# Kernel optimization log

Hardware: AMD Instinct MI355X
Metric: run time of the kernel (lower is better)

The kernel has to match this reference:

```python
import jax, jax.numpy as jnp
import numpy as np

TOP_K = 8


def setup_inputs() -> dict:
    key = jax.random.key(0)
    ks = jax.random.split(key, 10)
    B, N, F = 16, 4096, 256
    M = 4096  # memory_size
    s = 1.0 / np.sqrt(F)
    return {
        "query": jax.random.normal(ks[0], (B, N, F), jnp.float32),
        "memory_keys": jax.random.normal(ks[1], (M, F), jnp.float32),
        "memory_values": jax.random.normal(ks[2], (M, F), jnp.float32),
        "Wq": jax.random.normal(ks[3], (F, F), jnp.float32) * s,
        "bq": jnp.zeros((F,), jnp.float32),
        "W1": jax.random.normal(ks[4], (2 * F, F), jnp.float32) * (1.0 / np.sqrt(2 * F)),
        "b1": jnp.zeros((F,), jnp.float32),
        "W2": jax.random.normal(ks[5], (F, F), jnp.float32) * s,
        "b2": jnp.zeros((F,), jnp.float32),
    }


def reference(query, memory_keys, memory_values, Wq, bq, W1, b1, W2, b2):
    # query: (B, N, F)
    q = jnp.einsum("bnf,fg->bng", query, Wq) + bq
    # similarity vs memory bank: (B, N, M)
    sim = jnp.einsum("bnf,mf->bnm", q, memory_keys)
    topk_sim, topk_idx = jax.lax.top_k(sim, TOP_K)          # (B, N, K)
    topk_values = memory_values[topk_idx]                    # (B, N, K, F) gather
    weights = jax.nn.softmax(topk_sim, axis=-1)[..., None]   # (B, N, K, 1)
    retrieved = jnp.sum(topk_values * weights, axis=-2)      # (B, N, F)
    h = jnp.concatenate([query, retrieved], axis=-1)         # (B, N, 2F)
    h = jax.nn.relu(jnp.einsum("bnf,fg->bng", h, W1) + b1)
    out = jnp.einsum("bnf,fg->bng", h, W2) + b2
    return out
```

## Files before the change

### kernel.cpp

```cpp
#include <hip/hip_runtime.h>

typedef _Float16 f16x8 __attribute__((ext_vector_type(8)));
typedef _Float16 f16x4 __attribute__((ext_vector_type(4)));
typedef float f32x4 __attribute__((ext_vector_type(4)));

#define BN   65536
#define MSZ  4096
#define TOPK 8

#define MFMA(a, b, c) __builtin_amdgcn_mfma_f32_16x16x32_f16(a, b, c, 0, 0, 0)

__global__ void cvt_f16(const float* __restrict__ src, _Float16* __restrict__ dst,
                        int n) {
    int i = blockIdx.x * 256 + threadIdx.x;
    if (i < n) dst[i] = (_Float16)src[i];
}

__global__ void cvt_transpose(const float* __restrict__ src, _Float16* __restrict__ dst,
                              int K, int N) {
    int i = blockIdx.x * 256 + threadIdx.x;
    if (i < K * N) {
        int k = i / N, n = i - k * N;
        dst[n * K + k] = (_Float16)src[i];
    }
}

__device__ __forceinline__ unsigned pack_key(float s, unsigned inv12) {
    unsigned u = __float_as_uint(s);
    unsigned m = (unsigned)(((int)u) >> 31) | 0x80000000u;
    unsigned k = u ^ m;
    return (k & 0xFFFFF000u) | inv12;
}

__device__ __forceinline__ unsigned med3u(unsigned a, unsigned b, unsigned c) {
    unsigned d;
    asm("v_med3_u32 %0, %1, %2, %3" : "=v"(d) : "v"(a), "v"(b), "v"(c));
    return d;
}

template <int N>
__device__ __forceinline__ void ins(unsigned* t, unsigned key) {
#pragma unroll
    for (int p = N - 1; p > 0; --p) t[p] = med3u(t[p - 1], t[p], key);
    t[0] = (t[0] > key) ? t[0] : key;
}

__device__ __forceinline__ int swz(int r, int cb) {
    return (r << 9) + (cb ^ ((r & 7) << 4));
}

__global__ __launch_bounds__(256, 2) void fused_all(
        const float*    __restrict__ query,
        const _Float16* __restrict__ keysH,
        const float*    __restrict__ vals,
        const _Float16* __restrict__ WqT,
        const float*    __restrict__ bq,
        const _Float16* __restrict__ W1T,
        const float*    __restrict__ b1,
        const _Float16* __restrict__ W2T,
        const float*    __restrict__ b2,
        float* __restrict__ out)
{
    __shared__ __attribute__((aligned(16))) unsigned char SM[65536];
    unsigned char* const SA = SM;
    unsigned char* const SB = SM + 32768;

    const int tid  = threadIdx.x;
    const int lane = tid & 63, quad = lane >> 4, l16 = lane & 15, wave = tid >> 6;
    const size_t row0 = (size_t)blockIdx.x * 64;

#pragma unroll
    for (int j = 0; j < 8; ++j) {
        int u = (j << 8) + tid;
        int r = u >> 5, f = (u & 31) << 3;
        float4 x = *(const float4*)(query + (row0 + r) * 256 + f);
        float4 y = *(const float4*)(query + (row0 + r) * 256 + f + 4);
        f16x8 h = {(_Float16)x.x, (_Float16)x.y, (_Float16)x.z, (_Float16)x.w,
                   (_Float16)y.x, (_Float16)y.y, (_Float16)y.z, (_Float16)y.w};
        *(f16x8*)(SA + swz(r, f << 1)) = h;
    }
    __syncthreads();

    {
        f32x4 acc[4][4];
#pragma unroll
        for (int rt = 0; rt < 4; ++rt)
#pragma unroll
            for (int nt = 0; nt < 4; ++nt)
                acc[rt][nt] = (f32x4){0.f, 0.f, 0.f, 0.f};
#pragma unroll
        for (int kf = 0; kf < 8; ++kf) {
            f16x8 a[4];
#pragma unroll
            for (int rt = 0; rt < 4; ++rt)
                a[rt] = *(const f16x8*)(SA + swz(rt * 16 + l16, kf * 64 + quad * 16));
#pragma unroll
            for (int nt = 0; nt < 4; ++nt) {
                int n0 = wave * 16 + nt * 64;
                f16x8 b = *(const f16x8*)(WqT + (size_t)(n0 + l16) * 256 + kf * 32 + quad * 8);
#pragma unroll
                for (int rt = 0; rt < 4; ++rt)
                    acc[rt][nt] = MFMA(a[rt], b, acc[rt][nt]);
            }
        }
#pragma unroll
        for (int nt = 0; nt < 4; ++nt) {
            int col = wave * 16 + nt * 64 + l16;
            float bv = bq[col];
#pragma unroll
            for (int rt = 0; rt < 4; ++rt)
#pragma unroll
                for (int r = 0; r < 4; ++r) {
                    int row = rt * 16 + quad * 4 + r;
                    *(_Float16*)(SB + swz(row, col * 2)) =
                        (_Float16)(acc[rt][nt][r] + bv);
                }
        }
    }
    __syncthreads();

    f16x8 af[8];
    {
        f16x8 kst[8];
#pragma unroll
        for (int j = 0; j < 8; ++j) {
            int u = (j << 8) + tid;
            int r = u >> 5, cb = (u & 31) << 4;
            kst[j] = *(const f16x8*)((const unsigned char*)keysH + (r << 9) + cb);
        }
#pragma unroll
        for (int nk = 0; nk < 8; ++nk)
            af[nk] = *(const f16x8*)(SB + swz(wave * 16 + l16, nk * 64 + quad * 16));
#pragma unroll
        for (int j = 0; j < 8; ++j) {
            int u = (j << 8) + tid;
            int r = u >> 5, cb = (u & 31) << 4;
            *(f16x8*)(SA + swz(r, cb)) = kst[j];
        }
    }
    __syncthreads();

    unsigned tk[4][7];
#pragma unroll
    for (int s = 0; s < 4; ++s)
#pragma unroll
        for (int e = 0; e < 7; ++e) tk[s][e] = 0u;

#pragma unroll 1
    for (int t = 0; t < 64; ++t) {
        const int cbase = (t & 1) << 15;
        const int nbase = 32768 - cbase;
        const unsigned char* ktg =
            (const unsigned char*)keysH + ((size_t)((t + 1) & 63) << 15);
        f16x8 kst[8];
#pragma unroll
        for (int j = 0; j < 8; ++j) {
            int u = (j << 8) + tid;
            int r = u >> 5, cb = (u & 31) << 4;
            kst[j] = *(const f16x8*)(ktg + (r << 9) + cb);
        }
        const unsigned char* KB = SM + cbase;
#pragma unroll
        for (int n0 = 0; n0 < 64; n0 += 16) {
            f16x8 bf[8];
#pragma unroll
            for (int nk = 0; nk < 8; ++nk)
                bf[nk] = *(const f16x8*)(KB + swz(n0 + l16, nk * 64 + quad * 16));
            f32x4 acc = {0.f, 0.f, 0.f, 0.f};
#pragma unroll
            for (int nk = 0; nk < 8; ++nk) acc = MFMA(af[nk], bf[nk], acc);
            unsigned inv = (~(unsigned)((t << 6) + n0 + l16)) & 0xFFFu;
#pragma unroll
            for (int r = 0; r < 4; ++r) ins<7>(tk[r], pack_key(acc[r], inv));
        }
#pragma unroll
        for (int j = 0; j < 8; ++j) {
            int u = (j << 8) + tid;
            int r = u >> 5, cb = (u & 31) << 4;
            *(f16x8*)(SM + nbase + swz(r, cb)) = kst[j];
        }
        __syncthreads();
    }

    unsigned t8[2][8];
    {
        const int kh = l16 & 1;
#pragma unroll
        for (int j = 0; j < 2; ++j) {
#pragma unroll
            for (int e = 0; e < 7; ++e) t8[j][e] = kh ? tk[2 + j][e] : tk[j][e];
            t8[j][7] = 0u;
        }
#pragma unroll
        for (int j = 0; j < 2; ++j)
#pragma unroll
            for (int e = 0; e < 7; ++e) {
                unsigned snd = kh ? tk[j][e] : tk[2 + j][e];
                unsigned rcv = __shfl_xor(snd, 1);
                ins<8>(t8[j], rcv);
            }
    }
    unsigned keep[8];
    {
        const int k2 = (l16 >> 1) & 1;
        unsigned oth[8];
#pragma unroll
        for (int e = 0; e < 8; ++e) {
            keep[e] = k2 ? t8[1][e] : t8[0][e];
            oth[e]  = k2 ? t8[0][e] : t8[1][e];
        }
#pragma unroll
        for (int e = 0; e < 8; ++e) ins<8>(keep, __shfl_xor(oth[e], 2));
    }
#pragma unroll
    for (int st = 4; st <= 8; st <<= 1) {
        unsigned rcv[8];
#pragma unroll
        for (int e = 0; e < 8; ++e) rcv[e] = __shfl_xor(keep[e], st);
#pragma unroll
        for (int e = 0; e < 8; ++e) ins<8>(keep, rcv[e]);
    }

    int idx[8];
    {
        const int src = ((l16 >> 2) << 4) + (((l16 & 1) << 1) | ((l16 >> 1) & 1));
#pragma unroll
        for (int e = 0; e < 8; ++e) {
            unsigned kb = __shfl(keep[e], src);
            idx[e] = 4095 - (int)(kb & 0xFFFu);
        }
    }

    float wt[8];
    {
        float ps[8];
#pragma unroll
        for (int e = 0; e < 8; ++e) {
            const f16x8* kp = (const f16x8*)(keysH + (size_t)(idx[e] & (MSZ - 1)) * 256);
            float s = 0.f;
#pragma unroll
            for (int nk = 0; nk < 8; ++nk) {
                f16x8 kv = kp[nk * 4 + quad];
                f16x8 qv = af[nk];
#pragma unroll
                for (int i = 0; i < 8; ++i) s += (float)qv[i] * (float)kv[i];
            }
            ps[e] = s;
        }
#pragma unroll
        for (int e = 0; e < 8; ++e) {
            ps[e] += __shfl_xor(ps[e], 16);
            ps[e] += __shfl_xor(ps[e], 32);
        }
        float mx = ps[0];
#pragma unroll
        for (int e = 1; e < 8; ++e) mx = fmaxf(mx, ps[e]);
        float z = 0.f;
#pragma unroll
        for (int e = 0; e < 8; ++e) { wt[e] = __expf(ps[e] - mx); z += wt[e]; }
        float rz = 1.f / z;
#pragma unroll
        for (int e = 0; e < 8; ++e) wt[e] *= rz;
    }

    {
        float rv[64];
#pragma unroll
        for (int i = 0; i < 64; ++i) rv[i] = 0.f;
#pragma unroll
        for (int e = 0; e < 8; ++e) {
            const float4* vp = (const float4*)(vals + (size_t)(idx[e] & (MSZ - 1)) * 256 + quad * 64);
            float w = wt[e];
#pragma unroll
            for (int j = 0; j < 16; ++j) {
                float4 v = vp[j];
                rv[j * 4 + 0] += w * v.x; rv[j * 4 + 1] += w * v.y;
                rv[j * 4 + 2] += w * v.z; rv[j * 4 + 3] += w * v.w;
            }
        }
#pragma unroll
        for (int j = 0; j < 8; ++j) {
            f16x8 h = {(_Float16)rv[j * 8 + 0], (_Float16)rv[j * 8 + 1],
                       (_Float16)rv[j * 8 + 2], (_Float16)rv[j * 8 + 3],
                       (_Float16)rv[j * 8 + 4], (_Float16)rv[j * 8 + 5],
                       (_Float16)rv[j * 8 + 6], (_Float16)rv[j * 8 + 7]};
            *(f16x8*)(SB + swz(wave * 16 + l16, quad * 128 + (j << 4))) = h;
        }
    }
#pragma unroll
    for (int j = 0; j < 8; ++j) {
        int u = (j << 8) + tid;
        int r = u >> 5, f = (u & 31) << 3;
        float4 x = *(const float4*)(query + (row0 + r) * 256 + f);
        float4 y = *(const float4*)(query + (row0 + r) * 256 + f + 4);
        f16x8 h = {(_Float16)x.x, (_Float16)x.y, (_Float16)x.z, (_Float16)x.w,
                   (_Float16)y.x, (_Float16)y.y, (_Float16)y.z, (_Float16)y.w};
        *(f16x8*)(SA + swz(r, f << 1)) = h;
    }
    __syncthreads();

    {
        f32x4 acc[4][4];
#pragma unroll
        for (int rt = 0; rt < 4; ++rt)
#pragma unroll
            for (int nt = 0; nt < 4; ++nt)
                acc[rt][nt] = (f32x4){0.f, 0.f, 0.f, 0.f};
#pragma unroll
        for (int kf = 0; kf < 16; ++kf) {
            const unsigned char* base = (kf < 8) ? SA : SB;
            const int cb = (kf & 7) * 64 + quad * 16;
            f16x8 a[4];
#pragma unroll
            for (int rt = 0; rt < 4; ++rt)
                a[rt] = *(const f16x8*)(base + swz(rt * 16 + l16, cb));
#pragma unroll
            for (int nt = 0; nt < 4; ++nt) {
                int n0 = wave * 16 + nt * 64;
                f16x8 b = *(const f16x8*)(W1T + (size_t)(n0 + l16) * 512 + kf * 32 + quad * 8);
#pragma unroll
                for (int rt = 0; rt < 4; ++rt)
                    acc[rt][nt] = MFMA(a[rt], b, acc[rt][nt]);
            }
        }
        __syncthreads();
#pragma unroll
        for (int nt = 0; nt < 4; ++nt) {
            int col = wave * 16 + nt * 64 + l16;
            float bv = b1[col];
#pragma unroll
            for (int rt = 0; rt < 4; ++rt)
#pragma unroll
                for (int r = 0; r < 4; ++r) {
                    int row = rt * 16 + quad * 4 + r;
                    *(_Float16*)(SA + swz(row, col * 2)) =
                        (_Float16)fmaxf(acc[rt][nt][r] + bv, 0.f);
                }
        }
    }
    __syncthreads();

    {
        f32x4 acc[4][4];
#pragma unroll
        for (int rt = 0; rt < 4; ++rt)
#pragma unroll
            for (int nt = 0; nt < 4; ++nt)
                acc[rt][nt] = (f32x4){0.f, 0.f, 0.f, 0.f};
#pragma unroll
        for (int kf = 0; kf < 8; ++kf) {
            f16x8 a[4];
#pragma unroll
            for (int rt = 0; rt < 4; ++rt)
                a[rt] = *(const f16x8*)(SA + swz(rt * 16 + l16, kf * 64 + quad * 16));
#pragma unroll
            for (int nt = 0; nt < 4; ++nt) {
                int n0 = wave * 16 + nt * 64;
                f16x8 b = *(const f16x8*)(W2T + (size_t)(n0 + l16) * 256 + kf * 32 + quad * 8);
#pragma unroll
                for (int rt = 0; rt < 4; ++rt)
                    acc[rt][nt] = MFMA(a[rt], b, acc[rt][nt]);
            }
        }
#pragma unroll
        for (int nt = 0; nt < 4; ++nt) {
            int col = wave * 16 + nt * 64 + l16;
            float bv = b2[col];
#pragma unroll
            for (int rt = 0; rt < 4; ++rt)
#pragma unroll
                for (int r = 0; r < 4; ++r)
                    out[(row0 + rt * 16 + quad * 4 + r) * 256 + col] =
                        acc[rt][nt][r] + bv;
        }
    }
}

extern "C" void kernel_launch(void* const* d_in, const int* in_sizes, int n_in,
                              void* d_out, int out_size, void* d_ws, size_t ws_size,
                              hipStream_t stream) {
    const float* query = (const float*)d_in[0];
    const float* keys  = (const float*)d_in[1];
    const float* vals  = (const float*)d_in[2];
    const float* Wq    = (const float*)d_in[3];
    const float* bq    = (const float*)d_in[4];
    const float* W1    = (const float*)d_in[5];
    const float* b1    = (const float*)d_in[6];
    const float* W2    = (const float*)d_in[7];
    const float* b2    = (const float*)d_in[8];
    float* out = (float*)d_out;

    char* ws = (char*)d_ws;
    _Float16* keysH = (_Float16*)(ws);
    _Float16* WqT   = (_Float16*)(ws + 2097152);
    _Float16* W1T   = (_Float16*)(ws + 2097152 + 131072);
    _Float16* W2T   = (_Float16*)(ws + 2097152 + 131072 + 262144);

    cvt_f16<<<4096, 256, 0, stream>>>(keys, keysH, MSZ * 256);
    cvt_transpose<<<256, 256, 0, stream>>>(Wq, WqT, 256, 256);
    cvt_transpose<<<512, 256, 0, stream>>>(W1, W1T, 512, 256);
    cvt_transpose<<<256, 256, 0, stream>>>(W2, W2T, 256, 256);

    fused_all<<<BN / 64, 256, 0, stream>>>(query, keysH, vals, WqT, bq,
                                           W1T, b1, W2T, b2, out);
}
```

Before: 538.4 us.

## Pre-swizzle keys, stream tiles via global_load_lds, retile similarity per wave

```diff
diff --git a/kernel.cpp b/kernel.cpp
--- a/kernel.cpp
+++ b/kernel.cpp
@@ -1,7 +1,6 @@
 #include <hip/hip_runtime.h>
 
 typedef _Float16 f16x8 __attribute__((ext_vector_type(8)));
-typedef _Float16 f16x4 __attribute__((ext_vector_type(4)));
 typedef float f32x4 __attribute__((ext_vector_type(4)));
 
 #define BN   65536
@@ -10,18 +9,35 @@
 
 #define MFMA(a, b, c) __builtin_amdgcn_mfma_f32_16x16x32_f16(a, b, c, 0, 0, 0)
 
-__global__ void cvt_f16(const float* __restrict__ src, _Float16* __restrict__ dst,
-                        int n) {
-    int i = blockIdx.x * 256 + threadIdx.x;
-    if (i < n) dst[i] = (_Float16)src[i];
-}
-
-__global__ void cvt_transpose(const float* __restrict__ src, _Float16* __restrict__ dst,
-                              int K, int N) {
-    int i = blockIdx.x * 256 + threadIdx.x;
-    if (i < K * N) {
-        int k = i / N, n = i - k * N;
-        dst[n * K + k] = (_Float16)src[i];
+__device__ __forceinline__ int swz2(int r, int cb) {
+    return (r << 9) + (cb ^ ((((r >> 3) ^ r) & 7) << 4));
+}
+
+__global__ void prep(const float* __restrict__ keys, _Float16* __restrict__ keysSW,
+                     const float* __restrict__ Wq, _Float16* __restrict__ WqT,
+                     const float* __restrict__ W1, _Float16* __restrict__ W1T,
+                     const float* __restrict__ W2, _Float16* __restrict__ W2T) {
+    const int b = blockIdx.x, tid = threadIdx.x;
+    if (b < 512) {
+        int g = b * 256 + tid;
+        int k = g >> 5, f8 = g & 31;
+        float4 x = *(const float4*)(keys + (size_t)k * 256 + f8 * 8);
+        float4 y = *(const float4*)(keys + (size_t)k * 256 + f8 * 8 + 4);
+        f16x8 h = {(_Float16)x.x, (_Float16)x.y, (_Float16)x.z, (_Float16)x.w,
+                   (_Float16)y.x, (_Float16)y.y, (_Float16)y.z, (_Float16)y.w};
+        *(f16x8*)((char*)keysSW + ((size_t)(k >> 6) << 15) + swz2(k & 63, f8 * 16)) = h;
+    } else if (b < 768) {
+        int i = (b - 512) * 256 + tid;
+        int kk = i >> 8, n = i & 255;
+        WqT[n * 256 + kk] = (_Float16)Wq[i];
+    } else if (b < 1280) {
+        int i = (b - 768) * 256 + tid;
+        int kk = i >> 8, n = i & 255;
+        W1T[n * 512 + kk] = (_Float16)W1[i];
+    } else {
+        int i = (b - 1280) * 256 + tid;
+        int kk = i >> 8, n = i & 255;
+        W2T[n * 256 + kk] = (_Float16)W2[i];
     }
 }
 
@@ -45,13 +61,15 @@
     t[0] = (t[0] > key) ? t[0] : key;
 }
 
-__device__ __forceinline__ int swz(int r, int cb) {
-    return (r << 9) + (cb ^ ((r & 7) << 4));
+__device__ __forceinline__ void load_lds16(const void* g, void* l) {
+    __builtin_amdgcn_global_load_lds(
+        (const __attribute__((address_space(1))) unsigned int*)g,
+        (__attribute__((address_space(3))) unsigned int*)l, 16, 0, 0);
 }
 
 __global__ __launch_bounds__(256, 2) void fused_all(
         const float*    __restrict__ query,
-        const _Float16* __restrict__ keysH,
+        const _Float16* __restrict__ keysSW,
         const float*    __restrict__ vals,
         const _Float16* __restrict__ WqT,
         const float*    __restrict__ bq,
@@ -77,7 +95,7 @@
         float4 y = *(const float4*)(query + (row0 + r) * 256 + f + 4);
         f16x8 h = {(_Float16)x.x, (_Float16)x.y, (_Float16)x.z, (_Float16)x.w,
                    (_Float16)y.x, (_Float16)y.y, (_Float16)y.z, (_Float16)y.w};
-        *(f16x8*)(SA + swz(r, f << 1)) = h;
+        *(f16x8*)(SA + swz2(r, f << 1)) = h;
     }
     __syncthreads();
 
@@ -93,7 +111,7 @@
             f16x8 a[4];
 #pragma unroll
             for (int rt = 0; rt < 4; ++rt)
-                a[rt] = *(const f16x8*)(SA + swz(rt * 16 + l16, kf * 64 + quad * 16));
+                a[rt] = *(const f16x8*)(SA + swz2(rt * 16 + l16, kf * 64 + quad * 16));
 #pragma unroll
             for (int nt = 0; nt < 4; ++nt) {
                 int n0 = wave * 16 + nt * 64;
@@ -112,136 +130,159 @@
 #pragma unroll
                 for (int r = 0; r < 4; ++r) {
                     int row = rt * 16 + quad * 4 + r;
-                    *(_Float16*)(SB + swz(row, col * 2)) =
+                    *(_Float16*)(SB + swz2(row, col * 2)) =
                         (_Float16)(acc[rt][nt][r] + bv);
                 }
         }
     }
     __syncthreads();
 
-    f16x8 af[8];
-    {
-        f16x8 kst[8];
-#pragma unroll
-        for (int j = 0; j < 8; ++j) {
-            int u = (j << 8) + tid;
-            int r = u >> 5, cb = (u & 31) << 4;
-            kst[j] = *(const f16x8*)((const unsigned char*)keysH + (r << 9) + cb);
-        }
-#pragma unroll
-        for (int nk = 0; nk < 8; ++nk)
-            af[nk] = *(const f16x8*)(SB + swz(wave * 16 + l16, nk * 64 + quad * 16));
-#pragma unroll
-        for (int j = 0; j < 8; ++j) {
-            int u = (j << 8) + tid;
-            int r = u >> 5, cb = (u & 31) << 4;
-            *(f16x8*)(SA + swz(r, cb)) = kst[j];
-        }
-    }
-    __syncthreads();
-
-    unsigned tk[4][7];
-#pragma unroll
-    for (int s = 0; s < 4; ++s)
-#pragma unroll
-        for (int e = 0; e < 7; ++e) tk[s][e] = 0u;
+    f16x8 af0[8], af1[8];
+    {
+        const char* src = (const char*)keysSW + wave * 8192;
+        char* dst = (char*)SA + wave * 8192;
+#pragma unroll
+        for (int j = 0; j < 8; ++j)
+            load_lds16(src + j * 1024 + lane * 16, dst + j * 1024);
+#pragma unroll
+        for (int nk = 0; nk < 8; ++nk) {
+            af0[nk] = *(const f16x8*)(SB + swz2((wave & 1) * 32 + l16,      nk * 64 + quad * 16));
+            af1[nk] = *(const f16x8*)(SB + swz2((wave & 1) * 32 + 16 + l16, nk * 64 + quad * 16));
+        }
+    }
+    __syncthreads();
+
+    unsigned tk[8][6];
+#pragma unroll
+    for (int s = 0; s < 8; ++s)
+#pragma unroll
+        for (int e = 0; e < 6; ++e) tk[s][e] = 0u;
+
+    const int kh = (wave >> 1) * 32;
 
 #pragma unroll 1
     for (int t = 0; t < 64; ++t) {
-        const int cbase = (t & 1) << 15;
-        const int nbase = 32768 - cbase;
-        const unsigned char* ktg =
-            (const unsigned char*)keysH + ((size_t)((t + 1) & 63) << 15);
-        f16x8 kst[8];
-#pragma unroll
-        for (int j = 0; j < 8; ++j) {
-            int u = (j << 8) + tid;
-            int r = u >> 5, cb = (u & 31) << 4;
-            kst[j] = *(const f16x8*)(ktg + (r << 9) + cb);
-        }
-        const unsigned char* KB = SM + cbase;
-#pragma unroll
-        for (int n0 = 0; n0 < 64; n0 += 16) {
+        unsigned char* cur = SM + ((t & 1) << 15);
+        unsigned char* nxt = SM + (((t + 1) & 1) << 15);
+        {
+            const char* src = (const char*)keysSW + ((size_t)((t + 1) & 63) << 15) + wave * 8192;
+            char* dst = (char*)nxt + wave * 8192;
+#pragma unroll
+            for (int j = 0; j < 8; ++j)
+                load_lds16(src + j * 1024 + lane * 16, dst + j * 1024);
+        }
+#pragma unroll
+        for (int c = 0; c < 2; ++c) {
+            const int kl = kh + c * 16;
             f16x8 bf[8];
 #pragma unroll
             for (int nk = 0; nk < 8; ++nk)
-                bf[nk] = *(const f16x8*)(KB + swz(n0 + l16, nk * 64 + quad * 16));
-            f32x4 acc = {0.f, 0.f, 0.f, 0.f};
-#pragma unroll
-            for (int nk = 0; nk < 8; ++nk) acc = MFMA(af[nk], bf[nk], acc);
-            unsigned inv = (~(unsigned)((t << 6) + n0 + l16)) & 0xFFFu;
-#pragma unroll
-            for (int r = 0; r < 4; ++r) ins<7>(tk[r], pack_key(acc[r], inv));
-        }
-#pragma unroll
-        for (int j = 0; j < 8; ++j) {
-            int u = (j << 8) + tid;
-            int r = u >> 5, cb = (u & 31) << 4;
-            *(f16x8*)(SM + nbase + swz(r, cb)) = kst[j];
+                bf[nk] = *(const f16x8*)(cur + swz2(kl + l16, nk * 64 + quad * 16));
+            f32x4 a0 = {0.f, 0.f, 0.f, 0.f};
+            f32x4 a1 = {0.f, 0.f, 0.f, 0.f};
+#pragma unroll
+            for (int nk = 0; nk < 8; ++nk) {
+                a0 = MFMA(af0[nk], bf[nk], a0);
+                a1 = MFMA(af1[nk], bf[nk], a1);
+            }
+            unsigned inv = (~(unsigned)((t << 6) + kl + l16)) & 0xFFFu;
+#pragma unroll
+            for (int r = 0; r < 4; ++r) ins<6>(tk[r],     pack_key(a0[r], inv));
+#pragma unroll
+            for (int r = 0; r < 4; ++r) ins<6>(tk[4 + r], pack_key(a1[r], inv));
         }
         __syncthreads();
     }
 
-    unsigned t8[2][8];
-    {
-        const int kh = l16 & 1;
+    unsigned m4[4][7];
+    {
+        const int kb = l16 & 1;
+#pragma unroll
+        for (int j = 0; j < 4; ++j) {
+#pragma unroll
+            for (int e = 0; e < 6; ++e) m4[j][e] = kb ? tk[4 + j][e] : tk[j][e];
+            m4[j][6] = 0u;
+#pragma unroll
+            for (int e = 0; e < 6; ++e) {
+                unsigned snd = kb ? tk[j][e] : tk[4 + j][e];
+                ins<7>(m4[j], __shfl_xor(snd, 1));
+            }
+        }
+    }
+    unsigned m2[2][8];
+    {
+        const int k2 = (l16 >> 1) & 1;
 #pragma unroll
         for (int j = 0; j < 2; ++j) {
 #pragma unroll
-            for (int e = 0; e < 7; ++e) t8[j][e] = kh ? tk[2 + j][e] : tk[j][e];
-            t8[j][7] = 0u;
-        }
-#pragma unroll
-        for (int j = 0; j < 2; ++j)
+            for (int e = 0; e < 7; ++e) m2[j][e] = k2 ? m4[2 + j][e] : m4[j][e];
+            m2[j][7] = 0u;
 #pragma unroll
             for (int e = 0; e < 7; ++e) {
-                unsigned snd = kh ? tk[j][e] : tk[2 + j][e];
-                unsigned rcv = __shfl_xor(snd, 1);
-                ins<8>(t8[j], rcv);
-            }
-    }
-    unsigned keep[8];
-    {
-        const int k2 = (l16 >> 1) & 1;
+                unsigned snd = k2 ? m4[j][e] : m4[2 + j][e];
+                ins<8>(m2[j], __shfl_xor(snd, 2));
+            }
+        }
+    }
+    unsigned fm[8];
+    {
+        const int k3 = (l16 >> 2) & 1;
         unsigned oth[8];
 #pragma unroll
         for (int e = 0; e < 8; ++e) {
-            keep[e] = k2 ? t8[1][e] : t8[0][e];
-            oth[e]  = k2 ? t8[0][e] : t8[1][e];
-        }
-#pragma unroll
-        for (int e = 0; e < 8; ++e) ins<8>(keep, __shfl_xor(oth[e], 2));
-    }
-#pragma unroll
-    for (int st = 4; st <= 8; st <<= 1) {
+            fm[e]  = k3 ? m2[1][e] : m2[0][e];
+            oth[e] = k3 ? m2[0][e] : m2[1][e];
+        }
+#pragma unroll
+        for (int e = 0; e < 8; ++e) ins<8>(fm, __shfl_xor(oth[e], 4));
+    }
+    {
         unsigned rcv[8];
 #pragma unroll
-        for (int e = 0; e < 8; ++e) rcv[e] = __shfl_xor(keep[e], st);
-#pragma unroll
-        for (int e = 0; e < 8; ++e) ins<8>(keep, rcv[e]);
-    }
-
+        for (int e = 0; e < 8; ++e) rcv[e] = __shfl_xor(fm[e], 8);
+#pragma unroll
+        for (int e = 0; e < 8; ++e) ins<8>(fm, rcv[e]);
+    }
+    if (l16 < 8) {
+        const int rl  = quad * 4 + 2 * ((l16 >> 1) & 1) + ((l16 >> 2) & 1) + 16 * (l16 & 1);
+        const int row = (wave & 1) * 32 + rl;
+        unsigned* Mrg = (unsigned*)SA;
+#pragma unroll
+        for (int e = 0; e < 8; ++e) Mrg[((wave >> 1) * 64 + row) * 8 + e] = fm[e];
+    }
+    __syncthreads();
+
+    const int rmap = ((wave & 1) << 5) + ((wave & 2) << 3);
     int idx[8];
     {
-        const int src = ((l16 >> 2) << 4) + (((l16 & 1) << 1) | ((l16 >> 1) & 1));
+        const unsigned* Mrg = (const unsigned*)SA;
+        const int row = rmap + l16;
+        unsigned f[8];
+#pragma unroll
+        for (int e = 0; e < 8; ++e) f[e] = Mrg[row * 8 + e];
+#pragma unroll
+        for (int e = 0; e < 8; ++e) ins<8>(f, Mrg[(64 + row) * 8 + e]);
+#pragma unroll
+        for (int e = 0; e < 8; ++e) idx[e] = 4095 - (int)(f[e] & 0xFFFu);
+    }
+
+    float wt[8];
+    {
+        f16x8 afr[8];
+        const bool hi = (wave & 2) != 0;
+#pragma unroll
+        for (int nk = 0; nk < 8; ++nk) afr[nk] = hi ? af1[nk] : af0[nk];
+        float ps[8];
 #pragma unroll
         for (int e = 0; e < 8; ++e) {
-            unsigned kb = __shfl(keep[e], src);
-            idx[e] = 4095 - (int)(kb & 0xFFFu);
-        }
-    }
-
-    float wt[8];
-    {
-        float ps[8];
-#pragma unroll
-        for (int e = 0; e < 8; ++e) {
-            const f16x8* kp = (const f16x8*)(keysH + (size_t)(idx[e] & (MSZ - 1)) * 256);
+            const unsigned char* kb =
+                (const unsigned char*)keysSW + ((size_t)(idx[e] >> 6) << 15);
+            const int kr = idx[e] & 63;
             float s = 0.f;
 #pragma unroll
             for (int nk = 0; nk < 8; ++nk) {
-                f16x8 kv = kp[nk * 4 + quad];
-                f16x8 qv = af[nk];
+                f16x8 kv = *(const f16x8*)(kb + swz2(kr, nk * 64 + quad * 16));
+                f16x8 qv = afr[nk];
 #pragma unroll
                 for (int i = 0; i < 8; ++i) s += (float)qv[i] * (float)kv[i];
             }
@@ -278,15 +319,18 @@
                 rv[j * 4 + 2] += w * v.z; rv[j * 4 + 3] += w * v.w;
             }
         }
+        const int row = rmap + l16;
 #pragma unroll
         for (int j = 0; j < 8; ++j) {
             f16x8 h = {(_Float16)rv[j * 8 + 0], (_Float16)rv[j * 8 + 1],
                        (_Float16)rv[j * 8 + 2], (_Float16)rv[j * 8 + 3],
                        (_Float16)rv[j * 8 + 4], (_Float16)rv[j * 8 + 5],
                        (_Float16)rv[j * 8 + 6], (_Float16)rv[j * 8 + 7]};
-            *(f16x8*)(SB + swz(wave * 16 + l16, quad * 128 + (j << 4))) = h;
-        }
-    }
+            *(f16x8*)(SB + swz2(row, quad * 128 + (j << 4))) = h;
+        }
+    }
+    __syncthreads();
+
 #pragma unroll
     for (int j = 0; j < 8; ++j) {
         int u = (j << 8) + tid;
@@ -295,7 +339,7 @@
         float4 y = *(const float4*)(query + (row0 + r) * 256 + f + 4);
         f16x8 h = {(_Float16)x.x, (_Float16)x.y, (_Float16)x.z, (_Float16)x.w,
                    (_Float16)y.x, (_Float16)y.y, (_Float16)y.z, (_Float16)y.w};
-        *(f16x8*)(SA + swz(r, f << 1)) = h;
+        *(f16x8*)(SA + swz2(r, f << 1)) = h;
     }
     __syncthreads();
 
@@ -313,7 +357,7 @@
             f16x8 a[4];
 #pragma unroll
             for (int rt = 0; rt < 4; ++rt)
-                a[rt] = *(const f16x8*)(base + swz(rt * 16 + l16, cb));
+                a[rt] = *(const f16x8*)(base + swz2(rt * 16 + l16, cb));
 #pragma unroll
             for (int nt = 0; nt < 4; ++nt) {
                 int n0 = wave * 16 + nt * 64;
@@ -333,7 +377,7 @@
 #pragma unroll
                 for (int r = 0; r < 4; ++r) {
                     int row = rt * 16 + quad * 4 + r;
-                    *(_Float16*)(SA + swz(row, col * 2)) =
+                    *(_Float16*)(SA + swz2(row, col * 2)) =
                         (_Float16)fmaxf(acc[rt][nt][r] + bv, 0.f);
                 }
         }
@@ -352,7 +396,7 @@
             f16x8 a[4];
 #pragma unroll
             for (int rt = 0; rt < 4; ++rt)
-                a[rt] = *(const f16x8*)(SA + swz(rt * 16 + l16, kf * 64 + quad * 16));
+                a[rt] = *(const f16x8*)(SA + swz2(rt * 16 + l16, kf * 64 + quad * 16));
 #pragma unroll
             for (int nt = 0; nt < 4; ++nt) {
                 int n0 = wave * 16 + nt * 64;
@@ -391,16 +435,13 @@
     float* out = (float*)d_out;
 
     char* ws = (char*)d_ws;
-    _Float16* keysH = (_Float16*)(ws);
-    _Float16* WqT   = (_Float16*)(ws + 2097152);
-    _Float16* W1T   = (_Float16*)(ws + 2097152 + 131072);
-    _Float16* W2T   = (_Float16*)(ws + 2097152 + 131072 + 262144);
-
-    cvt_f16<<<4096, 256, 0, stream>>>(keys, keysH, MSZ * 256);
-    cvt_transpose<<<256, 256, 0, stream>>>(Wq, WqT, 256, 256);
-    cvt_transpose<<<512, 256, 0, stream>>>(W1, W1T, 512, 256);
-    cvt_transpose<<<256, 256, 0, stream>>>(W2, W2T, 256, 256);
-
-    fused_all<<<BN / 64, 256, 0, stream>>>(query, keysH, vals, WqT, bq,
+    _Float16* keysSW = (_Float16*)(ws);
+    _Float16* WqT    = (_Float16*)(ws + 2097152);
+    _Float16* W1T    = (_Float16*)(ws + 2097152 + 131072);
+    _Float16* W2T    = (_Float16*)(ws + 2097152 + 131072 + 262144);
+
+    prep<<<1536, 256, 0, stream>>>(keys, keysSW, Wq, WqT, W1, W1T, W2, W2T);
+
+    fused_all<<<BN / 64, 256, 0, stream>>>(query, keysSW, vals, WqT, bq,
                                            W1T, b1, W2T, b2, out);
 }
```

New measurement: 484.7 us. 10.0% less time.
